# Kernel optimization log

Measured on AMD Instinct MI355X. Metric: run time of the kernel, lower is better.

Reference implementation:

```python
import jax, jax.numpy as jnp
import numpy as np

B, S, HID = 2, 2048, 2048
NH, NKV, HD = 16, 4, 128
ROT = 64            # head_dim * partial_rotary_factor
WINDOW = 512        # sliding_window_size
ROPE_BASE = 10000.0


def setup_inputs() -> dict:
    key = jax.random.key(0)
    ks = jax.random.split(key, 5)
    scale = 0.02
    return {
        "hidden_states": jax.random.normal(ks[0], (B, S, HID), jnp.float32),
        "Wq": jax.random.normal(ks[1], (NH * HD, HID), jnp.float32) * scale,
        "Wk": jax.random.normal(ks[2], (NKV * HD, HID), jnp.float32) * scale,
        "Wv": jax.random.normal(ks[3], (NKV * HD, HID), jnp.float32) * scale,
        "Wo": jax.random.normal(ks[4], (HID, NH * HD), jnp.float32) * scale,
    }


def _rope_cos_sin(seq_len, dtype):
    inv_freq = 1.0 / (ROPE_BASE ** (jnp.arange(0, ROT, 2, dtype=jnp.float32) / ROT))
    t = jnp.arange(seq_len, dtype=jnp.float32)
    freqs = t[:, None] * inv_freq[None, :]          # [S, ROT/2]
    emb = jnp.concatenate([freqs, freqs], axis=-1)   # [S, ROT]
    return jnp.cos(emb).astype(dtype), jnp.sin(emb).astype(dtype)


def _rotate_half(x):
    x1, x2 = x[..., : x.shape[-1] // 2], x[..., x.shape[-1] // 2:]
    return jnp.concatenate([-x2, x1], axis=-1)


def reference(hidden_states, Wq, Wk, Wv, Wo):
    b, s, _ = hidden_states.shape
    n_rep = NH // NKV

    q = (hidden_states @ Wq.T).reshape(b, s, NH, HD).transpose(0, 2, 1, 3)    # [B,NH,S,HD]
    k = (hidden_states @ Wk.T).reshape(b, s, NKV, HD).transpose(0, 2, 1, 3)   # [B,NKV,S,HD]
    v = (hidden_states @ Wv.T).reshape(b, s, NKV, HD).transpose(0, 2, 1, 3)

    # partial rotary embedding on the first ROT dims
    cos, sin = _rope_cos_sin(s, q.dtype)   # [S, ROT]
    cos = cos[None, None]                  # broadcast over batch, heads
    sin = sin[None, None]
    q_rot, q_pass = q[..., :ROT], q[..., ROT:]
    k_rot, k_pass = k[..., :ROT], k[..., ROT:]
    q_rot = q_rot * cos + _rotate_half(q_rot) * sin
    k_rot = k_rot * cos + _rotate_half(k_rot) * sin
    q = jnp.concatenate([q_rot, q_pass], axis=-1)
    k = jnp.concatenate([k_rot, k_pass], axis=-1)

    # GQA: repeat kv heads
    k = jnp.repeat(k, n_rep, axis=1)   # [B,NH,S,HD]
    v = jnp.repeat(v, n_rep, axis=1)

    scores = jnp.einsum("bhqd,bhkd->bhqk", q, k) / jnp.sqrt(jnp.asarray(HD, q.dtype))

    # sliding-window causal mask: allow j in [i-WINDOW+1, i]
    i = jnp.arange(s)[:, None]
    j = jnp.arange(s)[None, :]
    allowed = (j <= i) & (j > i - WINDOW)
    scores = jnp.where(allowed[None, None], scores, -jnp.inf)

    attn = jax.nn.softmax(scores.astype(jnp.float32), axis=-1).astype(q.dtype)
    out = jnp.einsum("bhqk,bhkd->bhqd", attn, v)          # [B,NH,S,HD]
    out = out.transpose(0, 2, 1, 3).reshape(b, s, NH * HD)
    return out @ Wo.T
```

## Files before the change

kernel.cpp:

```cpp
#include <hip/hip_runtime.h>
#include <cstdint>
#include <cstddef>

typedef __bf16 bf16;
typedef __attribute__((ext_vector_type(8))) __bf16 bf16x8;
typedef __attribute__((ext_vector_type(4))) __bf16 bf16x4;
typedef __attribute__((ext_vector_type(4))) float f32x4;
typedef __attribute__((ext_vector_type(4))) short s16x4;

#define S_LEN   2048
#define WIN     512
#define NH_Q    16
#define NH_KV   4
#define HD_     128
#define NTOK    4096

#if defined(__has_builtin)
#if __has_builtin(__builtin_amdgcn_mfma_f32_16x16x16bf16_1k)
#define HAVE_MFMA16 1
#endif
#endif
#ifndef HAVE_MFMA16
#define HAVE_MFMA16 0
#endif

#define WAIT_VM40  0x8F78
#define WAIT_VM20  0x4F74
#define WAIT_VM0   0x0F70
#define WAIT_LGKM0 0xC07F
#define CFENCE() __asm__ __volatile__("" ::: "memory")

__device__ __forceinline__ void async_copy16(const void* g, void* l) {
  __builtin_amdgcn_global_load_lds(
      (const __attribute__((address_space(1))) void*)g,
      (__attribute__((address_space(3))) void*)l, 16, 0, 0);
}

__global__ __launch_bounds__(256)
void cvt_all(const float* __restrict__ hs, const float* __restrict__ wq,
             const float* __restrict__ wk, const float* __restrict__ wv,
             const float* __restrict__ wo, bf16* __restrict__ hsb,
             bf16* __restrict__ wqb, bf16* __restrict__ wkb,
             bf16* __restrict__ wvb, bf16* __restrict__ wob) {
  long i = ((long)blockIdx.x * 256 + threadIdx.x) * 4;
  const float* in;
  bf16* out;
  if (i < 8388608)       { in = hs + i;            out = hsb + i; }
  else if (i < 12582912) { in = wq + (i - 8388608); out = wqb + (i - 8388608); }
  else if (i < 13631488) { in = wk + (i - 12582912); out = wkb + (i - 12582912); }
  else if (i < 14680064) { in = wv + (i - 13631488); out = wvb + (i - 13631488); }
  else                   { in = wo + (i - 14680064); out = wob + (i - 14680064); }
  float4 v = *(const float4*)in;
  bf16x4 t = {(bf16)v.x, (bf16)v.y, (bf16)v.z, (bf16)v.w};
  *(bf16x4*)out = t;
}

template <typename OutT>
__global__ __launch_bounds__(256)
void gemm_bt(const bf16* __restrict__ A, const bf16* __restrict__ W,
             OutT* __restrict__ C, int M, int N, int K) {
  __shared__ __align__(16) bf16 As[2][128 * 32];
  __shared__ __align__(16) bf16 Bs[2][128 * 32];
  const int tid  = threadIdx.x;
  const int wave = tid >> 6, lane = tid & 63;
  const int quad = lane >> 4, l16 = lane & 15;
  const int wm = wave >> 1, wn = wave & 1;
  const int m0 = blockIdx.y * 128, n0 = blockIdx.x * 128;
  const int lrow = lane >> 2;
  const int lcol = (((lane & 3) + ((lane >> 3) & 3)) & 3) * 8;
  const int gfrag = ((quad - ((l16 >> 1) & 3)) & 3) * 8;

  f32x4 acc[4][4];
#pragma unroll
  for (int i = 0; i < 4; ++i)
#pragma unroll
    for (int j = 0; j < 4; ++j) acc[i][j] = (f32x4){0.f, 0.f, 0.f, 0.f};

  auto stage = [&](int buf, int k0) {
#pragma unroll
    for (int it = 0; it < 2; ++it) {
      const int c   = it * 4 + wave;
      const int row = c * 16 + lrow;
      async_copy16(A + (size_t)(m0 + row) * K + k0 + lcol, &As[buf][c * 512]);
      async_copy16(W + (size_t)(n0 + row) * K + k0 + lcol, &Bs[buf][c * 512]);
    }
  };

  stage(0, 0);
  __syncthreads();
  for (int k0 = 0; k0 < K; k0 += 32) {
    const int cur = (k0 >> 5) & 1;
    if (k0 + 32 < K) stage(cur ^ 1, k0 + 32);
    bf16x8 af[4], bfr[4];
#pragma unroll
    for (int mt = 0; mt < 4; ++mt)
      af[mt] = *(const bf16x8*)&As[cur][(wm * 64 + mt * 16 + l16) * 32 + gfrag];
#pragma unroll
    for (int nt = 0; nt < 4; ++nt)
      bfr[nt] = *(const bf16x8*)&Bs[cur][(wn * 64 + nt * 16 + l16) * 32 + gfrag];
#pragma unroll
    for (int mt = 0; mt < 4; ++mt)
#pragma unroll
      for (int nt = 0; nt < 4; ++nt)
        acc[mt][nt] = __builtin_amdgcn_mfma_f32_16x16x32_bf16(
            af[mt], bfr[nt], acc[mt][nt], 0, 0, 0);
    __syncthreads();
  }
#pragma unroll
  for (int mt = 0; mt < 4; ++mt)
#pragma unroll
    for (int nt = 0; nt < 4; ++nt)
#pragma unroll
      for (int r = 0; r < 4; ++r) {
        const int row = m0 + wm * 64 + mt * 16 + quad * 4 + r;
        const int col = n0 + wn * 64 + nt * 16 + l16;
        C[(size_t)row * N + col] = (OutT)acc[mt][nt][r];
      }
}

__global__ __launch_bounds__(448, 4)
void gemm_qkv(const bf16* __restrict__ A, const bf16* __restrict__ Wq,
              const bf16* __restrict__ Wk, const bf16* __restrict__ Wv,
              bf16* __restrict__ Qo, bf16* __restrict__ Ko,
              bf16* __restrict__ Vt) {
  __shared__ __align__(16) bf16 As[3][128 * 32];
  __shared__ __align__(16) bf16 Bs[3][192 * 32];
  __shared__ int ready[3];
  __shared__ int done[3];
  const int tid = threadIdx.x, wave = tid >> 6, lane = tid & 63;
  const int quad = lane >> 4, l16 = lane & 15;
  const int bx = blockIdx.x;
  const int m0 = blockIdx.y * 128;
  if (tid < 3) ready[tid] = 0;
  else if (tid < 6) done[tid - 3] = 0;
  __syncthreads();
  volatile int* vready = ready;
  volatile int* vdone  = done;
  const int R = 64;

  if (wave == 6) {
    const int lrow = lane >> 2;
    const int lcol = (((lane & 3) + ((lane >> 3) & 3)) & 3) * 8;
    const bf16* arow = A + (size_t)(m0 + lrow) * 2048 + lcol;
    const bf16* brow[12];
#pragma unroll
    for (int c = 0; c < 12; ++c) {
      const int n = bx * 192 + c * 16 + lrow;
      brow[c] = (n < 2048 ? Wq + (size_t)n * 2048
               : n < 2560 ? Wk + (size_t)(n - 2048) * 2048
                          : Wv + (size_t)(n - 2560) * 2048) + lcol;
    }
    int slot = 0, pslot = 0, need = 0;
    for (int g = 0; g < R; ++g) {
      if (slot == 0 && g) need += 6;
      while (vdone[slot] < need) __builtin_amdgcn_s_sleep(1);
      const int k0 = g * 32;
#pragma unroll
      for (int c = 0; c < 8; ++c)
        async_copy16(arow + (size_t)c * 16 * 2048 + k0, &As[slot][c * 512]);
#pragma unroll
      for (int c = 0; c < 12; ++c)
        async_copy16(brow[c] + k0, &Bs[slot][c * 512]);
      __builtin_amdgcn_s_waitcnt(WAIT_VM40);
      if (g >= 2) {
        if (lane == 0) vready[pslot] = g - 1;
        pslot = pslot == 2 ? 0 : pslot + 1;
      }
      slot = slot == 2 ? 0 : slot + 1;
    }
    __builtin_amdgcn_s_waitcnt(WAIT_VM20);
    if (lane == 0) vready[pslot] = R - 1;
    pslot = pslot == 2 ? 0 : pslot + 1;
    __builtin_amdgcn_s_waitcnt(WAIT_VM0);
    if (lane == 0) vready[pslot] = R;
    return;
  }

  const int wm = wave / 3, wn = wave % 3;
  const int gfrag = ((quad - ((l16 >> 1) & 3)) & 3) * 8;
  f32x4 acc[4][4];
#pragma unroll
  for (int i = 0; i < 4; ++i)
#pragma unroll
    for (int j = 0; j < 4; ++j) acc[i][j] = (f32x4){0.f, 0.f, 0.f, 0.f};

  int slot = 0;
  for (int g = 0; g < R; ++g) {
    while (vready[slot] < g + 1) __builtin_amdgcn_s_sleep(1);
    CFENCE();
    bf16x8 af[4], bfr[4];
#pragma unroll
    for (int mt = 0; mt < 4; ++mt)
      af[mt] = *(const bf16x8*)&As[slot][(wm * 64 + mt * 16 + l16) * 32 + gfrag];
#pragma unroll
    for (int nt = 0; nt < 4; ++nt)
      bfr[nt] = *(const bf16x8*)&Bs[slot][(wn * 64 + nt * 16 + l16) * 32 + gfrag];
#pragma unroll
    for (int mt = 0; mt < 4; ++mt)
#pragma unroll
      for (int nt = 0; nt < 4; ++nt)
        acc[mt][nt] = __builtin_amdgcn_mfma_f32_16x16x32_bf16(
            af[mt], bfr[nt], acc[mt][nt], 0, 0, 0);
    __builtin_amdgcn_s_waitcnt(WAIT_LGKM0);
    CFENCE();
    if (lane == 0) atomicAdd(&done[slot], 1);
    slot = slot == 2 ? 0 : slot + 1;
  }

  const int cbase = bx * 192 + wn * 64;
  if (cbase < 2560 && (cbase & 127) == 0) {
#pragma unroll
    for (int nt = 0; nt < 2; ++nt) {
      const int d = nt * 16 + l16;
      const float invf = exp2f(-(float)d * 0.41524101186091903f);
#pragma unroll
      for (int mt = 0; mt < 4; ++mt)
#pragma unroll
        for (int r = 0; r < 4; ++r) {
          const int pos = (m0 + wm * 64 + mt * 16 + quad * 4 + r) & (S_LEN - 1);
          float s, c;
          __sincosf((float)pos * invf, &s, &c);
          const float x1 = acc[mt][nt][r], x2 = acc[mt][nt + 2][r];
          acc[mt][nt][r]     = x1 * c - x2 * s;
          acc[mt][nt + 2][r] = x2 * c + x1 * s;
        }
    }
  }
#pragma unroll
  for (int mt = 0; mt < 4; ++mt) {
    const int row0 = m0 + wm * 64 + mt * 16 + quad * 4;
#pragma unroll
    for (int nt = 0; nt < 4; ++nt) {
      const int col16 = cbase + nt * 16;
      if (col16 < 2048) {
#pragma unroll
        for (int r = 0; r < 4; ++r)
          Qo[(size_t)(row0 + r) * 2048 + col16 + l16] = (bf16)acc[mt][nt][r];
      } else if (col16 < 2560) {
#pragma unroll
        for (int r = 0; r < 4; ++r)
          Ko[(size_t)(row0 + r) * 512 + col16 - 2048 + l16] = (bf16)acc[mt][nt][r];
      } else {
        const int colv = col16 + l16 - 2560;
        const int b = row0 >> 11, s0 = row0 & (S_LEN - 1);
        bf16x4 t = {(bf16)acc[mt][nt][0], (bf16)acc[mt][nt][1],
                    (bf16)acc[mt][nt][2], (bf16)acc[mt][nt][3]};
        *(bf16x4*)(Vt + ((size_t)(b * NH_KV + (colv >> 7)) * HD_ + (colv & 127))
                        * S_LEN + s0) = t;
      }
    }
  }
}

#define KS_STRIDE 136
#define VT_STRIDE 72

__global__ __launch_bounds__(256)
void attn_kernel(const bf16* __restrict__ Qg, const bf16* __restrict__ Kg,
                 const bf16* __restrict__ Vtg, bf16* __restrict__ Og) {
  __shared__ __align__(16) bf16 Ks[64 * KS_STRIDE];
  __shared__ __align__(16) bf16 Vt[128 * VT_STRIDE];
#if !HAVE_MFMA16
  __shared__ __align__(16) bf16 Pb[4][16 * 72];
#endif
  const int tid  = threadIdx.x;
  const int wave = tid >> 6, lane = tid & 63;
  const int quad = lane >> 4, l16 = lane & 15;
  const int qt = blockIdx.x, h = blockIdx.y, b = blockIdx.z;
  const int kv = h >> 2;
  const int q0 = qt * 64;
  const int tok0 = b * S_LEN;
  const float scale = 0.08838834764831845f;
  const int q = q0 + wave * 16 + l16;

  bf16x8 qf[4];
  {
    const bf16* qp = Qg + (size_t)(tok0 + q) * (NH_Q * HD_) + h * HD_ + quad * 8;
#pragma unroll
    for (int kb = 0; kb < 4; ++kb) qf[kb] = *(const bf16x8*)(qp + kb * 32);
  }

  f32x4 o[8];
#pragma unroll
  for (int dt = 0; dt < 8; ++dt) o[dt] = (f32x4){0.f, 0.f, 0.f, 0.f};
  float m_run = -__builtin_inff(), l_run = 0.f;

  int kt_begin = q0 - WIN;
  if (kt_begin < 0) kt_begin = 0;
  const int kt_end = q0 + 64;
  const bf16* vt_base = Vtg + (size_t)(b * NH_KV + kv) * HD_ * S_LEN;

  for (int kt = kt_begin; kt < kt_end; kt += 64) {
    __syncthreads();
#pragma unroll
    for (int it = 0; it < 4; ++it) {
      int vid = tid + it * 256;
      int key = vid >> 4, dblk = vid & 15;
      bf16x8 v = *(const bf16x8*)(Kg + (size_t)(tok0 + kt + key) * (NH_KV * HD_)
                                  + kv * HD_ + dblk * 8);
      *(bf16x8*)&Ks[key * KS_STRIDE + dblk * 8] = v;
    }
#pragma unroll
    for (int it = 0; it < 4; ++it) {
      int vid = tid + it * 256;
      int d = vid >> 3, kblk = vid & 7;
      bf16x8 v = *(const bf16x8*)(vt_base + (size_t)d * S_LEN + kt + kblk * 8);
      *(bf16x8*)&Vt[d * VT_STRIDE + kblk * 8] = v;
    }
    __syncthreads();

    f32x4 st[4];
#pragma unroll
    for (int nt = 0; nt < 4; ++nt) {
      f32x4 acc = (f32x4){0.f, 0.f, 0.f, 0.f};
#pragma unroll
      for (int kb = 0; kb < 4; ++kb) {
        bf16x8 kf = *(const bf16x8*)&Ks[(nt * 16 + l16) * KS_STRIDE + kb * 32 + quad * 8];
        acc = __builtin_amdgcn_mfma_f32_16x16x32_bf16(kf, qf[kb], acc, 0, 0, 0);
      }
      st[nt] = acc;
    }
#pragma unroll
    for (int nt = 0; nt < 4; ++nt)
#pragma unroll
      for (int r = 0; r < 4; ++r) {
        int key = kt + nt * 16 + quad * 4 + r;
        bool ok = (key <= q) && (key > q - WIN);
        st[nt][r] = ok ? st[nt][r] * scale : -__builtin_inff();
      }
    float mx = -__builtin_inff();
#pragma unroll
    for (int nt = 0; nt < 4; ++nt)
#pragma unroll
      for (int r = 0; r < 4; ++r) mx = fmaxf(mx, st[nt][r]);
    mx = fmaxf(mx, __shfl_xor(mx, 16, 64));
    mx = fmaxf(mx, __shfl_xor(mx, 32, 64));
    float mnew = fmaxf(m_run, mx);
    float msub = (mnew == -__builtin_inff()) ? 0.f : mnew;
    float alpha = __expf(m_run - msub);
    m_run = mnew;
    float p[4][4], psum = 0.f;
#pragma unroll
    for (int nt = 0; nt < 4; ++nt)
#pragma unroll
      for (int r = 0; r < 4; ++r) {
        p[nt][r] = __expf(st[nt][r] - msub);
        psum += p[nt][r];
      }
    psum += __shfl_xor(psum, 16, 64);
    psum += __shfl_xor(psum, 32, 64);
    l_run = l_run * alpha + psum;
#pragma unroll
    for (int dt = 0; dt < 8; ++dt) o[dt] *= alpha;

#if HAVE_MFMA16
    s16x4 pb[4];
#pragma unroll
    for (int nt = 0; nt < 4; ++nt)
#pragma unroll
      for (int r = 0; r < 4; ++r) {
        union { __bf16 h; short s; } u;
        u.h = (bf16)p[nt][r];
        pb[nt][r] = u.s;
      }
#pragma unroll
    for (int dt = 0; dt < 8; ++dt)
#pragma unroll
      for (int nt = 0; nt < 4; ++nt) {
        s16x4 vf = *(const s16x4*)&Vt[(dt * 16 + l16) * VT_STRIDE + nt * 16 + quad * 4];
        o[dt] = __builtin_amdgcn_mfma_f32_16x16x16bf16_1k(vf, pb[nt], o[dt], 0, 0, 0);
      }
#else
#pragma unroll
    for (int nt = 0; nt < 4; ++nt) {
      bf16x4 t;
#pragma unroll
      for (int r = 0; r < 4; ++r) t[r] = (bf16)p[nt][r];
      *(bf16x4*)&Pb[wave][l16 * 72 + nt * 16 + quad * 4] = t;
    }
    __syncthreads();
    bf16x8 pf[2];
    pf[0] = *(const bf16x8*)&Pb[wave][l16 * 72 + quad * 8];
    pf[1] = *(const bf16x8*)&Pb[wave][l16 * 72 + 32 + quad * 8];
#pragma unroll
    for (int dt = 0; dt < 8; ++dt)
#pragma unroll
      for (int kb = 0; kb < 2; ++kb) {
        bf16x8 vf = *(const bf16x8*)&Vt[(dt * 16 + l16) * VT_STRIDE + kb * 32 + quad * 8];
        o[dt] = __builtin_amdgcn_mfma_f32_16x16x32_bf16(vf, pf[kb], o[dt], 0, 0, 0);
      }
#endif
  }

  float inv = 1.f / l_run;
  __syncthreads();
#pragma unroll
  for (int dt = 0; dt < 8; ++dt) {
    bf16x4 t;
#pragma unroll
    for (int r = 0; r < 4; ++r) t[r] = (bf16)(o[dt][r] * inv);
    *(bf16x4*)&Ks[(wave * 16 + l16) * KS_STRIDE + dt * 16 + quad * 4] = t;
  }
  __syncthreads();
#pragma unroll
  for (int it = 0; it < 4; ++it) {
    int idx = tid + it * 256;
    int row = idx >> 4, chunk = idx & 15;
    bf16x8 v = *(const bf16x8*)&Ks[row * KS_STRIDE + chunk * 8];
    *(bf16x8*)(Og + (size_t)(tok0 + q0 + row) * (NH_Q * HD_) + h * HD_ + chunk * 8) = v;
  }
}

extern "C" void kernel_launch(void* const* d_in, const int* in_sizes, int n_in,
                              void* d_out, int out_size, void* d_ws, size_t ws_size,
                              hipStream_t stream) {
  const float* hs = (const float*)d_in[0];
  const float* Wq = (const float*)d_in[1];
  const float* Wk = (const float*)d_in[2];
  const float* Wv = (const float*)d_in[3];
  const float* Wo = (const float*)d_in[4];
  float* out = (float*)d_out;

  char* w = (char*)d_ws;
  bf16* hsb = (bf16*)w; w += (size_t)NTOK * 2048 * 2;
  bf16* wqb = (bf16*)w; w += (size_t)2048 * 2048 * 2;
  bf16* wkb = (bf16*)w; w += (size_t)512 * 2048 * 2;
  bf16* wvb = (bf16*)w; w += (size_t)512 * 2048 * 2;
  bf16* wob = (bf16*)w; w += (size_t)2048 * 2048 * 2;
  bf16* qb  = (bf16*)w; w += (size_t)NTOK * 2048 * 2;
  bf16* kb  = (bf16*)w; w += (size_t)NTOK * 512 * 2;
  bf16* vtb = (bf16*)w; w += (size_t)NTOK * 512 * 2;
  bf16* ab  = hsb;

  cvt_all<<<18874368 / 1024, 256, 0, stream>>>(hs, Wq, Wk, Wv, Wo,
                                               hsb, wqb, wkb, wvb, wob);

  gemm_qkv<<<dim3(16, NTOK / 128), 448, 0, stream>>>(hsb, wqb, wkb, wvb,
                                                     qb, kb, vtb);

  attn_kernel<<<dim3(S_LEN / 64, NH_Q, 2), 256, 0, stream>>>(qb, kb, vtb, ab);

  gemm_bt<float><<<dim3(2048 / 128, NTOK / 128), 256, 0, stream>>>(
      ab, wob, out, NTOK, 2048, 2048);
}
```

Before: 277.2 us.

## Replace warp-specialized QKV GEMM with 8-wave 256x256 tile double-buffered kernel

The QKV projection GEMM moves from a 128x192 tile, where one producer wave feeds six consumer waves through shared-memory flags, to a 256x256 tile run by eight waves. Every wave issues its own async global-to-LDS copies into double-buffered, XOR-swizzled 64-wide K slices. Loads and MFMA quarters are interleaved with barriers, MFMA priority is raised with setprio, and block indices are swizzled for L2 locality. The aim is more operand reuse per byte loaded and removal of the spin-wait handshake overhead. The cost is 128KB of LDS per block, so far fewer blocks fit on each CU, and a grid of 192 blocks.

```diff
diff --git a/kernel.cpp b/kernel.cpp
--- a/kernel.cpp
+++ b/kernel.cpp
@@ -24,10 +24,9 @@
 #define HAVE_MFMA16 0
 #endif
 
-#define WAIT_VM40  0x8F78
-#define WAIT_VM20  0x4F74
+#define WAIT_VM4   0x0F74
+#define WAIT_VM2   0x0F72
 #define WAIT_VM0   0x0F70
-#define WAIT_LGKM0 0xC07F
 #define CFENCE() __asm__ __volatile__("" ::: "memory")
 
 __device__ __forceinline__ void async_copy16(const void* g, void* l) {
@@ -118,106 +117,159 @@
       }
 }
 
-__global__ __launch_bounds__(448, 4)
-void gemm_qkv(const bf16* __restrict__ A, const bf16* __restrict__ Wq,
-              const bf16* __restrict__ Wk, const bf16* __restrict__ Wv,
-              bf16* __restrict__ Qo, bf16* __restrict__ Ko,
-              bf16* __restrict__ Vt) {
-  __shared__ __align__(16) bf16 As[3][128 * 32];
-  __shared__ __align__(16) bf16 Bs[3][192 * 32];
-  __shared__ int ready[3];
-  __shared__ int done[3];
-  const int tid = threadIdx.x, wave = tid >> 6, lane = tid & 63;
+__global__ __launch_bounds__(512, 2)
+void gemm_qkv8(const bf16* __restrict__ A, const bf16* __restrict__ Wq,
+               const bf16* __restrict__ Wk, const bf16* __restrict__ Wv,
+               bf16* __restrict__ Qo, bf16* __restrict__ Ko,
+               bf16* __restrict__ Vt) {
+  __shared__ __align__(16) char smem[131072];
+  const int tid  = threadIdx.x;
+  const int wave = tid >> 6, lane = tid & 63;
   const int quad = lane >> 4, l16 = lane & 15;
-  const int bx = blockIdx.x;
-  const int m0 = blockIdx.y * 128;
-  if (tid < 3) ready[tid] = 0;
-  else if (tid < 6) done[tid - 3] = 0;
-  __syncthreads();
-  volatile int* vready = ready;
-  volatile int* vdone  = done;
-  const int R = 64;
-
-  if (wave == 6) {
-    const int lrow = lane >> 2;
-    const int lcol = (((lane & 3) + ((lane >> 3) & 3)) & 3) * 8;
-    const bf16* arow = A + (size_t)(m0 + lrow) * 2048 + lcol;
-    const bf16* brow[12];
-#pragma unroll
-    for (int c = 0; c < 12; ++c) {
-      const int n = bx * 192 + c * 16 + lrow;
-      brow[c] = (n < 2048 ? Wq + (size_t)n * 2048
-               : n < 2560 ? Wk + (size_t)(n - 2048) * 2048
-                          : Wv + (size_t)(n - 2560) * 2048) + lcol;
-    }
-    int slot = 0, pslot = 0, need = 0;
-    for (int g = 0; g < R; ++g) {
-      if (slot == 0 && g) need += 6;
-      while (vdone[slot] < need) __builtin_amdgcn_s_sleep(1);
-      const int k0 = g * 32;
-#pragma unroll
-      for (int c = 0; c < 8; ++c)
-        async_copy16(arow + (size_t)c * 16 * 2048 + k0, &As[slot][c * 512]);
-#pragma unroll
-      for (int c = 0; c < 12; ++c)
-        async_copy16(brow[c] + k0, &Bs[slot][c * 512]);
-      __builtin_amdgcn_s_waitcnt(WAIT_VM40);
-      if (g >= 2) {
-        if (lane == 0) vready[pslot] = g - 1;
-        pslot = pslot == 2 ? 0 : pslot + 1;
-      }
-      slot = slot == 2 ? 0 : slot + 1;
-    }
-    __builtin_amdgcn_s_waitcnt(WAIT_VM20);
-    if (lane == 0) vready[pslot] = R - 1;
-    pslot = pslot == 2 ? 0 : pslot + 1;
-    __builtin_amdgcn_s_waitcnt(WAIT_VM0);
-    if (lane == 0) vready[pslot] = R;
-    return;
-  }
-
-  const int wm = wave / 3, wn = wave % 3;
-  const int gfrag = ((quad - ((l16 >> 1) & 3)) & 3) * 8;
-  f32x4 acc[4][4];
-#pragma unroll
-  for (int i = 0; i < 4; ++i)
+  const int wm = wave >> 2, wn = wave & 3;
+
+  const int flat = blockIdx.y * 12 + blockIdx.x;
+  const int swz  = (flat & 7) * 24 + (flat >> 3);
+  const int m0 = (swz / 12) * 256;
+  const int n0 = (swz % 12) * 256;
+
+  const int rdb = (l16 * 64 + quad * 16) ^ ((l16 & 8) << 2);
+
+  const int srow = lane >> 2;
+  const int scol = ((lane & 3) * 8) ^ ((lane >> 5) << 4);
+  const bf16* asrc = A + (size_t)(m0 + srow) * 2048 + scol;
+  const bf16* aptr[2][2];
+  int adst[2][2];
+#pragma unroll
+  for (int mh = 0; mh < 2; ++mh)
+#pragma unroll
+    for (int j = 0; j < 2; ++j) {
+      const int rb = j * 8 + mh * 4 + (wave >> 1);
+      aptr[mh][j] = asrc + (size_t)rb * 16 * 2048 + (wave & 1) * 32;
+      adst[mh][j] = (rb * 2 + (wave & 1)) << 10;
+    }
+  const bf16* bptr[2][2];
+  int bdst[2][2];
+#pragma unroll
+  for (int nh = 0; nh < 2; ++nh)
+#pragma unroll
+    for (int j = 0; j < 2; ++j) {
+      const int rb = j * 8 + (wave >> 2) * 4 + nh * 2 + ((wave >> 1) & 1);
+      const int nrow = n0 + rb * 16 + srow;
+      const bf16* p = nrow < 2048 ? Wq + (size_t)nrow * 2048
+                    : nrow < 2560 ? Wk + (size_t)(nrow - 2048) * 2048
+                                  : Wv + (size_t)(nrow - 2560) * 2048;
+      bptr[nh][j] = p + scol + (wave & 1) * 32;
+      bdst[nh][j] = (rb * 2 + (wave & 1)) << 10;
+    }
+
+#define STAGE_A(mh, tt) do {                                        \
+    char* _b = smem + ((tt) & 1) * 32768;                           \
+    async_copy16(aptr[mh][0] + (tt) * 64, _b + adst[mh][0]);        \
+    async_copy16(aptr[mh][1] + (tt) * 64, _b + adst[mh][1]);        \
+  } while (0)
+#define STAGE_B(nh, tt) do {                                        \
+    char* _b = smem + 65536 + ((tt) & 1) * 32768;                   \
+    async_copy16(bptr[nh][0] + (tt) * 64, _b + bdst[nh][0]);        \
+    async_copy16(bptr[nh][1] + (tt) * 64, _b + bdst[nh][1]);        \
+  } while (0)
+
+  f32x4 acc[8][4];
+#pragma unroll
+  for (int i = 0; i < 8; ++i)
 #pragma unroll
     for (int j = 0; j < 4; ++j) acc[i][j] = (f32x4){0.f, 0.f, 0.f, 0.f};
 
-  int slot = 0;
-  for (int g = 0; g < R; ++g) {
-    while (vready[slot] < g + 1) __builtin_amdgcn_s_sleep(1);
-    CFENCE();
-    bf16x8 af[4], bfr[4];
+  bf16x8 afr[4][2];
+  bf16x8 bfr[2][2][2];
+
+  auto read_a = [&](const char* Ab, int mh) __attribute__((always_inline)) {
 #pragma unroll
     for (int mt = 0; mt < 4; ++mt)
-      af[mt] = *(const bf16x8*)&As[slot][(wm * 64 + mt * 16 + l16) * 32 + gfrag];
-#pragma unroll
-    for (int nt = 0; nt < 4; ++nt)
-      bfr[nt] = *(const bf16x8*)&Bs[slot][(wn * 64 + nt * 16 + l16) * 32 + gfrag];
+#pragma unroll
+      for (int ks = 0; ks < 2; ++ks)
+        afr[mt][ks] = *(const bf16x8*)(
+            Ab + (((wm * 8 + mh * 4 + mt) * 2 + ks) << 10) + rdb);
+  };
+  auto read_b = [&](const char* Bb, int nh) __attribute__((always_inline)) {
+#pragma unroll
+    for (int nt = 0; nt < 2; ++nt)
+#pragma unroll
+      for (int ks = 0; ks < 2; ++ks)
+        bfr[nh][nt][ks] = *(const bf16x8*)(
+            Bb + (((wn * 4 + nh * 2 + nt) * 2 + ks) << 10) + rdb);
+  };
+  auto do_mfma = [&](int mh, int nh) __attribute__((always_inline)) {
+    __builtin_amdgcn_s_setprio(1);
 #pragma unroll
     for (int mt = 0; mt < 4; ++mt)
 #pragma unroll
-      for (int nt = 0; nt < 4; ++nt)
-        acc[mt][nt] = __builtin_amdgcn_mfma_f32_16x16x32_bf16(
-            af[mt], bfr[nt], acc[mt][nt], 0, 0, 0);
-    __builtin_amdgcn_s_waitcnt(WAIT_LGKM0);
-    CFENCE();
-    if (lane == 0) atomicAdd(&done[slot], 1);
-    slot = slot == 2 ? 0 : slot + 1;
-  }
-
-  const int cbase = bx * 192 + wn * 64;
+      for (int nt = 0; nt < 2; ++nt)
+#pragma unroll
+        for (int ks = 0; ks < 2; ++ks)
+          acc[mh * 4 + mt][nh * 2 + nt] = __builtin_amdgcn_mfma_f32_16x16x32_bf16(
+              afr[mt][ks], bfr[nh][nt][ks], acc[mh * 4 + mt][nh * 2 + nt],
+              0, 0, 0);
+    __builtin_amdgcn_s_setprio(0);
+  };
+
+  STAGE_A(0, 0); STAGE_B(0, 0); STAGE_B(1, 0); STAGE_A(1, 0);
+  CFENCE();
+
+  for (int t = 0; t < 31; ++t) {
+    const char* Ab = smem + (t & 1) * 32768;
+    const char* Bb = smem + 65536 + (t & 1) * 32768;
+    const int nx = t + 1;
+    __builtin_amdgcn_s_waitcnt(WAIT_VM4); CFENCE();
+    __builtin_amdgcn_s_barrier(); CFENCE();
+    read_a(Ab, 0); read_b(Bb, 0);
+    STAGE_A(0, nx); CFENCE();
+    do_mfma(0, 0);
+    __builtin_amdgcn_s_waitcnt(WAIT_VM4); CFENCE();
+    __builtin_amdgcn_s_barrier(); CFENCE();
+    read_b(Bb, 1);
+    STAGE_B(0, nx); CFENCE();
+    do_mfma(0, 1);
+    __builtin_amdgcn_s_waitcnt(WAIT_VM4); CFENCE();
+    __builtin_amdgcn_s_barrier(); CFENCE();
+    read_a(Ab, 1);
+    STAGE_B(1, nx); CFENCE();
+    do_mfma(1, 0);
+    __builtin_amdgcn_s_barrier(); CFENCE();
+    STAGE_A(1, nx); CFENCE();
+    do_mfma(1, 1);
+  }
+  {
+    const char* Ab = smem + 32768;
+    const char* Bb = smem + 65536 + 32768;
+    __builtin_amdgcn_s_waitcnt(WAIT_VM4); CFENCE();
+    __builtin_amdgcn_s_barrier(); CFENCE();
+    read_a(Ab, 0); read_b(Bb, 0);
+    do_mfma(0, 0);
+    __builtin_amdgcn_s_waitcnt(WAIT_VM2); CFENCE();
+    __builtin_amdgcn_s_barrier(); CFENCE();
+    read_b(Bb, 1);
+    do_mfma(0, 1);
+    __builtin_amdgcn_s_waitcnt(WAIT_VM0); CFENCE();
+    __builtin_amdgcn_s_barrier(); CFENCE();
+    read_a(Ab, 1);
+    do_mfma(1, 0);
+    do_mfma(1, 1);
+  }
+#undef STAGE_A
+#undef STAGE_B
+
+  const int cbase = n0 + wn * 64;
   if (cbase < 2560 && (cbase & 127) == 0) {
 #pragma unroll
     for (int nt = 0; nt < 2; ++nt) {
       const int d = nt * 16 + l16;
       const float invf = exp2f(-(float)d * 0.41524101186091903f);
 #pragma unroll
-      for (int mt = 0; mt < 4; ++mt)
+      for (int mt = 0; mt < 8; ++mt)
 #pragma unroll
         for (int r = 0; r < 4; ++r) {
-          const int pos = (m0 + wm * 64 + mt * 16 + quad * 4 + r) & (S_LEN - 1);
+          const int pos = (m0 + wm * 128 + mt * 16 + quad * 4 + r) & (S_LEN - 1);
           float s, c;
           __sincosf((float)pos * invf, &s, &c);
           const float x1 = acc[mt][nt][r], x2 = acc[mt][nt + 2][r];
@@ -227,8 +279,8 @@
     }
   }
 #pragma unroll
-  for (int mt = 0; mt < 4; ++mt) {
-    const int row0 = m0 + wm * 64 + mt * 16 + quad * 4;
+  for (int mt = 0; mt < 8; ++mt) {
+    const int row0 = m0 + wm * 128 + mt * 16 + quad * 4;
 #pragma unroll
     for (int nt = 0; nt < 4; ++nt) {
       const int col16 = cbase + nt * 16;
@@ -243,10 +295,10 @@
       } else {
         const int colv = col16 + l16 - 2560;
         const int b = row0 >> 11, s0 = row0 & (S_LEN - 1);
-        bf16x4 t = {(bf16)acc[mt][nt][0], (bf16)acc[mt][nt][1],
-                    (bf16)acc[mt][nt][2], (bf16)acc[mt][nt][3]};
+        bf16x4 tq = {(bf16)acc[mt][nt][0], (bf16)acc[mt][nt][1],
+                     (bf16)acc[mt][nt][2], (bf16)acc[mt][nt][3]};
         *(bf16x4*)(Vt + ((size_t)(b * NH_KV + (colv >> 7)) * HD_ + (colv & 127))
-                        * S_LEN + s0) = t;
+                        * S_LEN + s0) = tq;
       }
     }
   }
@@ -435,8 +487,8 @@
   cvt_all<<<18874368 / 1024, 256, 0, stream>>>(hs, Wq, Wk, Wv, Wo,
                                                hsb, wqb, wkb, wvb, wob);
 
-  gemm_qkv<<<dim3(16, NTOK / 128), 448, 0, stream>>>(hsb, wqb, wkb, wvb,
-                                                     qb, kb, vtb);
+  gemm_qkv8<<<dim3(12, 16), 512, 0, stream>>>(hsb, wqb, wkb, wvb,
+                                              qb, kb, vtb);
 
   attn_kernel<<<dim3(S_LEN / 64, NH_Q, 2), 256, 0, stream>>>(qb, kb, vtb, ab);
 
```

After: 263.9 us. 1.05x faster.
